# Kernel tuning notes

Hardware: AMD Instinct MI355X
Metric: run time of the kernel (lower is better)

Reference implementation:

```python
import jax, jax.numpy as jnp
import numpy as np

N_QUBITS = 6

def _apply_1q(state, U, w):
    # state: [B] + [2]*6 complex; U: [2,2] complex
    ax = 1 + w
    s = jnp.moveaxis(state, ax, -1)
    s = jnp.einsum('...j,ij->...i', s, U)
    return jnp.moveaxis(s, -1, ax)

def _apply_cnot(state, ctrl, tgt):
    ca, ta = 1 + ctrl, 1 + tgt
    s = jnp.moveaxis(state, (ca, ta), (1, 2))  # [B,2,2,...]
    s = jnp.stack([s[:, 0], s[:, 1, ::-1]], axis=1)
    return jnp.moveaxis(s, (1, 2), (ca, ta))

def _rot(phi, theta, omega):
    # PennyLane Rot = RZ(omega) RY(theta) RZ(phi)
    c, s = jnp.cos(theta / 2), jnp.sin(theta / 2)
    return jnp.stack([
        jnp.stack([jnp.exp(-0.5j * (phi + omega)) * c, -jnp.exp(0.5j * (phi - omega)) * s]),
        jnp.stack([jnp.exp(-0.5j * (phi - omega)) * s, jnp.exp(0.5j * (phi + omega)) * c]),
    ])

def _quantum(xq, qw):
    B = xq.shape[0]
    # AngleEmbedding RY: product state, per-qubit amplitudes [cos(x/2), sin(x/2)]
    amps = jnp.stack([jnp.cos(xq / 2), jnp.sin(xq / 2)], axis=-1)  # [B,6,2]
    state = amps[:, 0]
    for i in range(1, N_QUBITS):
        state = jnp.einsum('b...,bj->b...j', state, amps[:, i])
    state = state.astype(jnp.complex64)  # [B,2,2,2,2,2,2]
    # StronglyEntanglingLayers: per layer Rot on each wire, then CNOT ring of range r
    n_layers = qw.shape[0]
    for l in range(n_layers):
        for w in range(N_QUBITS):
            U = _rot(qw[l, w, 0], qw[l, w, 1], qw[l, w, 2])
            state = _apply_1q(state, U, w)
        r = (l % (N_QUBITS - 1)) + 1  # default ranges
        for w in range(N_QUBITS):
            state = _apply_cnot(state, w, (w + r) % N_QUBITS)
    probs = jnp.abs(state) ** 2
    zs = []
    for w in range(N_QUBITS):
        axes = tuple(a for a in range(1, N_QUBITS + 1) if a != 1 + w)
        p = jnp.sum(probs, axis=axes)  # [B,2]
        zs.append(p[:, 0] - p[:, 1])
    return jnp.stack(zs, axis=-1)  # [B,6]

def setup_inputs() -> dict:
    key = jax.random.key(0)
    ks = jax.random.split(key, 10)
    B = 16384
    return {
        'xc': jax.random.normal(ks[0], (B, 2048), jnp.float32),
        'xq': jax.random.uniform(ks[1], (B, N_QUBITS), jnp.float32),
        'W1': jax.random.normal(ks[2], (64, 2048), jnp.float32) * 0.02,
        'b1': jnp.zeros((64,), jnp.float32),
        'qw': jax.random.uniform(ks[3], (3, N_QUBITS, 3), jnp.float32, 0.0, 2 * np.pi),
        'Wq': jax.random.normal(ks[4], (16, N_QUBITS), jnp.float32) * 0.3,
        'bq': jnp.zeros((16,), jnp.float32),
        'Wf': jax.random.normal(ks[5], (3, 80), jnp.float32) * 0.1,
        'bf': jnp.zeros((3,), jnp.float32),
    }

def reference(xc, xq, W1, b1, qw, Wq, bq, Wf, bf):
    c = jax.nn.relu(xc @ W1.T + b1)                 # [B,64]
    q = _quantum(xq, qw) @ Wq.T + bq                # [B,16]
    return jnp.concatenate([c, q], axis=1) @ Wf.T + bf  # [B,3]
```

## Files before the change

### kernel.cpp

```cpp
#include <hip/hip_runtime.h>
#include <hip/hip_bf16.h>

#define NQ 6

typedef __attribute__((ext_vector_type(8))) short short8;
typedef __attribute__((ext_vector_type(4))) float floatx4;

#define WS_MQ_F   8192
#define WS_CQ_F   (8192+18)
#define WS_W1BF_B 36864

__global__ __launch_bounds__(64) void prep_kernel(
    const float* __restrict__ qw, int n_layers,
    const float* __restrict__ W1, const float* __restrict__ Wq,
    const float* __restrict__ bq, const float* __restrict__ Wf,
    const float* __restrict__ bf, float* __restrict__ ws_f,
    short* __restrict__ w1bf)
{
    const int blk  = blockIdx.x;
    const int lane = threadIdx.x;

    if (blk == 0) {
        if (lane < 18) {
            int j = lane / 6, wi = lane % 6;
            float s = 0.f;
            for (int m = 0; m < 16; ++m) s += Wf[j*80 + 64 + m] * Wq[m*6 + wi];
            ws_f[WS_MQ_F + lane] = s;
        } else if (lane < 21) {
            int j = lane - 18;
            float s = bf[j];
            for (int m = 0; m < 16; ++m) s += Wf[j*80 + 64 + m] * bq[m];
            ws_f[WS_CQ_F + j] = s;
        }
    } else if (blk <= 64) {
        const int j = blk - 1;
        float re = (lane == j) ? 1.f : 0.f;
        float im = 0.f;
        for (int l = 0; l < n_layers; ++l) {
            for (int w = 0; w < NQ; ++w) {
                const float* g = qw + (l*NQ + w)*3;
                float phi = g[0], th = g[1], om = g[2];
                float c, s;  __sincosf(0.5f*th, &s, &c);
                float sa, ca; __sincosf(0.5f*(phi+om), &sa, &ca);
                float sb, cb; __sincosf(0.5f*(phi-om), &sb, &cb);
                float u00r =  c*ca, u00i = -c*sa;
                float u01r = -s*cb, u01i = -s*sb;
                float u10r =  s*cb, u10i = -s*sb;
                float u11r =  c*ca, u11i =  c*sa;
                int p = 5 - w, mask = 1 << p;
                float pre = __shfl_xor(re, mask, 64);
                float pim = __shfl_xor(im, mask, 64);
                int b = (lane >> p) & 1;
                float mr = b ? u11r : u00r, mi = b ? u11i : u00i;
                float pr = b ? u10r : u01r, pi = b ? u10i : u01i;
                float nre = mr*re - mi*im + pr*pre - pi*pim;
                float nim = mr*im + mi*re + pr*pim + pi*pre;
                re = nre; im = nim;
            }
            int r = l % (NQ-1) + 1;
            for (int w = 0; w < NQ; ++w) {
                int tgt = (w + r) % NQ;
                int tmask = 1 << (5 - tgt);
                float pre = __shfl_xor(re, tmask, 64);
                float pim = __shfl_xor(im, tmask, 64);
                int cs = (lane >> (5 - w)) & 1;
                re = cs ? pre : re;
                im = cs ? pim : im;
            }
        }
        ws_f[(lane*64 + j)*2 + 0] = re;
        ws_f[(lane*64 + j)*2 + 1] = im;
    } else {
        int idx = (blk - 65)*512 + lane*8;
        if (idx < 64*2048) {
            float4 a0 = *(const float4*)(W1 + idx);
            float4 a1 = *(const float4*)(W1 + idx + 4);
            union { short8 v; __hip_bfloat162 h[4]; } u;
            float2 f;
            f.x=a0.x; f.y=a0.y; u.h[0] = __float22bfloat162_rn(f);
            f.x=a0.z; f.y=a0.w; u.h[1] = __float22bfloat162_rn(f);
            f.x=a1.x; f.y=a1.y; u.h[2] = __float22bfloat162_rn(f);
            f.x=a1.z; f.y=a1.w; u.h[3] = __float22bfloat162_rn(f);
            *(short8*)(w1bf + idx) = u.v;
        }
    }
}

__global__ __launch_bounds__(256) void fused_kernel(
    const float* __restrict__ xq, const float2* __restrict__ U,
    const float* __restrict__ ws_f,
    const float* __restrict__ xc, const short* __restrict__ w1bf,
    const float* __restrict__ b1, const float* __restrict__ Wf,
    float* __restrict__ out)
{
    const int tid  = threadIdx.x;
    const int lane = tid & 63;
    const int t    = __builtin_amdgcn_readfirstlane((int)(tid >> 6));
    const int blk  = blockIdx.x;

    __shared__ float zbuf[4][64][6];
    __shared__ float qres[64][3];
    __shared__ float cl[64][65];

    {
        const int b = blk*64 + lane;
        float a[64];
        const float* x = xq + (size_t)b*6;
        a[0] = 1.f;
        #pragma unroll
        for (int q = 0; q < 6; ++q) {
            float c, s; __sincosf(0.5f*x[q], &s, &c);
            const int sz = 1 << q;
            #pragma unroll
            for (int m = sz-1; m >= 0; --m) {
                float v = a[m];
                a[2*m+1] = v*s;
                a[2*m+0] = v*c;
            }
        }

        float zp[6] = {0,0,0,0,0,0};
        const float2* Urow = U + t*16*64;
        for (int ii = 0; ii < 16; ++ii) {
            float rr = 0.f, ri = 0.f;
            #pragma unroll
            for (int j = 0; j < 64; ++j) {
                float2 u = Urow[ii*64 + j];
                rr += u.x * a[j];
                ri += u.y * a[j];
            }
            float p = rr*rr + ri*ri;
            int i = t*16 + ii;
            #pragma unroll
            for (int w = 0; w < 6; ++w) zp[w] += ((i >> (5-w)) & 1) ? -p : p;
        }
        #pragma unroll
        for (int w = 0; w < 6; ++w) zbuf[t][lane][w] = zp[w];
    }
    __syncthreads();
    if (t == 0) {
        float z[6];
        #pragma unroll
        for (int w = 0; w < 6; ++w)
            z[w] = zbuf[0][lane][w] + zbuf[1][lane][w] + zbuf[2][lane][w] + zbuf[3][lane][w];
        #pragma unroll
        for (int j = 0; j < 3; ++j) {
            float v = ws_f[WS_CQ_F + j];
            #pragma unroll
            for (int w = 0; w < 6; ++w) v += ws_f[WS_MQ_F + j*6 + w] * z[w];
            qres[lane][j] = v;
        }
    }

    const int row  = blk*64 + t*16 + (lane & 15);
    const int koff = (lane >> 4) * 8;

    const float* ap = xc + (size_t)row*2048 + koff;
    const short* bp = w1bf + (lane & 15)*2048 + koff;

    floatx4 acc0 = {0,0,0,0}, acc1 = {0,0,0,0}, acc2 = {0,0,0,0}, acc3 = {0,0,0,0};

    float4 a0  = *(const float4*)ap;
    float4 a1  = *(const float4*)(ap + 4);
    short8 b0  = *(const short8*)(bp);
    short8 bv1 = *(const short8*)(bp + 16*2048);
    short8 b2  = *(const short8*)(bp + 32*2048);
    short8 b3  = *(const short8*)(bp + 48*2048);

    #pragma unroll 4
    for (int kk = 1; kk < 64; ++kk) {
        const float* apn = ap + kk*32;
        const short* bpn = bp + kk*32;
        float4 na0 = *(const float4*)apn;
        float4 na1 = *(const float4*)(apn + 4);
        short8 nb0 = *(const short8*)(bpn);
        short8 nb1 = *(const short8*)(bpn + 16*2048);
        short8 nb2 = *(const short8*)(bpn + 32*2048);
        short8 nb3 = *(const short8*)(bpn + 48*2048);

        union { short8 v; __hip_bfloat162 h[4]; } af;
        float2 f;
        f.x=a0.x; f.y=a0.y; af.h[0] = __float22bfloat162_rn(f);
        f.x=a0.z; f.y=a0.w; af.h[1] = __float22bfloat162_rn(f);
        f.x=a1.x; f.y=a1.y; af.h[2] = __float22bfloat162_rn(f);
        f.x=a1.z; f.y=a1.w; af.h[3] = __float22bfloat162_rn(f);

        acc0 = __builtin_amdgcn_mfma_f32_16x16x32_bf16(af.v, b0,  acc0, 0, 0, 0);
        acc1 = __builtin_amdgcn_mfma_f32_16x16x32_bf16(af.v, bv1, acc1, 0, 0, 0);
        acc2 = __builtin_amdgcn_mfma_f32_16x16x32_bf16(af.v, b2,  acc2, 0, 0, 0);
        acc3 = __builtin_amdgcn_mfma_f32_16x16x32_bf16(af.v, b3,  acc3, 0, 0, 0);

        a0 = na0; a1 = na1; b0 = nb0; bv1 = nb1; b2 = nb2; b3 = nb3;
    }
    {
        union { short8 v; __hip_bfloat162 h[4]; } af;
        float2 f;
        f.x=a0.x; f.y=a0.y; af.h[0] = __float22bfloat162_rn(f);
        f.x=a0.z; f.y=a0.w; af.h[1] = __float22bfloat162_rn(f);
        f.x=a1.x; f.y=a1.y; af.h[2] = __float22bfloat162_rn(f);
        f.x=a1.z; f.y=a1.w; af.h[3] = __float22bfloat162_rn(f);
        acc0 = __builtin_amdgcn_mfma_f32_16x16x32_bf16(af.v, b0,  acc0, 0, 0, 0);
        acc1 = __builtin_amdgcn_mfma_f32_16x16x32_bf16(af.v, bv1, acc1, 0, 0, 0);
        acc2 = __builtin_amdgcn_mfma_f32_16x16x32_bf16(af.v, b2,  acc2, 0, 0, 0);
        acc3 = __builtin_amdgcn_mfma_f32_16x16x32_bf16(af.v, b3,  acc3, 0, 0, 0);
    }

    const int rbase = t*16 + ((lane >> 4) * 4);
    const int c0 = lane & 15;
    float bb0 = b1[c0], bb1 = b1[16 + c0], bb2 = b1[32 + c0], bb3 = b1[48 + c0];
    #pragma unroll
    for (int r = 0; r < 4; ++r) {
        cl[rbase + r][ 0 + c0] = fmaxf(acc0[r] + bb0, 0.f);
        cl[rbase + r][16 + c0] = fmaxf(acc1[r] + bb1, 0.f);
        cl[rbase + r][32 + c0] = fmaxf(acc2[r] + bb2, 0.f);
        cl[rbase + r][48 + c0] = fmaxf(acc3[r] + bb3, 0.f);
    }
    __syncthreads();

    const int rr2 = tid & 63;
    if (t < 3) {
        float v = 0.f;
        #pragma unroll
        for (int col = 0; col < 64; ++col) v += Wf[t*80 + col] * cl[rr2][col];
        int g = blk*64 + rr2;
        out[(size_t)g*3 + t] = v + qres[rr2][t];
    }
}

extern "C" void kernel_launch(void* const* d_in, const int* in_sizes, int n_in,
                              void* d_out, int out_size, void* d_ws, size_t ws_size,
                              hipStream_t stream) {
    const float* xc = (const float*)d_in[0];
    const float* xq = (const float*)d_in[1];
    const float* W1 = (const float*)d_in[2];
    const float* b1 = (const float*)d_in[3];
    const float* qw = (const float*)d_in[4];
    const float* Wq = (const float*)d_in[5];
    const float* bq = (const float*)d_in[6];
    const float* Wf = (const float*)d_in[7];
    const float* bf = (const float*)d_in[8];
    float* out = (float*)d_out;

    const int B = in_sizes[1] / NQ;
    const int n_layers = in_sizes[4] / (NQ * 3);

    char* ws = (char*)d_ws;
    float*  ws_f  = (float*)ws;
    float2* U     = (float2*)ws;
    short*  w1bf  = (short*)(ws + WS_W1BF_B);

    prep_kernel<<<dim3(321), dim3(64), 0, stream>>>(qw, n_layers, W1, Wq, bq, Wf, bf, ws_f, w1bf);
    fused_kernel<<<dim3(B/64), dim3(256), 0, stream>>>(xq, U, ws_f, xc, w1bf, b1, Wf, out);
}
```

Baseline: 245.2 us.

## Split fused kernel into 16 waves with one 16x16 MFMA tile each

Grows the fused block from 4 to 16 waves. The quantum statevector rows are split 4 per wave instead of 16, and the 64x64 linear-layer tile is split so each wave computes one 16x16 output tile with a single accumulator instead of four. With only 256 blocks, the aim is more resident waves per CU to hide load and MFMA latency and to shorten each wave's serial quantum loop. In exchange, each xc row slice is now loaded by four waves instead of one, relying on cache for reuse. The 1024-thread launch bound also caps registers per thread, which may spill the 64-float amplitude array.

```diff
diff --git a/kernel.cpp b/kernel.cpp
--- a/kernel.cpp
+++ b/kernel.cpp
@@ -86,7 +86,7 @@
     }
 }
 
-__global__ __launch_bounds__(256) void fused_kernel(
+__global__ __launch_bounds__(1024) void fused_kernel(
     const float* __restrict__ xq, const float2* __restrict__ U,
     const float* __restrict__ ws_f,
     const float* __restrict__ xc, const short* __restrict__ w1bf,
@@ -98,7 +98,7 @@
     const int t    = __builtin_amdgcn_readfirstlane((int)(tid >> 6));
     const int blk  = blockIdx.x;
 
-    __shared__ float zbuf[4][64][6];
+    __shared__ float zbuf[16][64][6];
     __shared__ float qres[64][3];
     __shared__ float cl[64][65];
 
@@ -120,8 +120,8 @@
         }
 
         float zp[6] = {0,0,0,0,0,0};
-        const float2* Urow = U + t*16*64;
-        for (int ii = 0; ii < 16; ++ii) {
+        const float2* Urow = U + t*4*64;
+        for (int ii = 0; ii < 4; ++ii) {
             float rr = 0.f, ri = 0.f;
             #pragma unroll
             for (int j = 0; j < 64; ++j) {
@@ -130,7 +130,7 @@
                 ri += u.y * a[j];
             }
             float p = rr*rr + ri*ri;
-            int i = t*16 + ii;
+            int i = t*4 + ii;
             #pragma unroll
             for (int w = 0; w < 6; ++w) zp[w] += ((i >> (5-w)) & 1) ? -p : p;
         }
@@ -141,8 +141,12 @@
     if (t == 0) {
         float z[6];
         #pragma unroll
-        for (int w = 0; w < 6; ++w)
-            z[w] = zbuf[0][lane][w] + zbuf[1][lane][w] + zbuf[2][lane][w] + zbuf[3][lane][w];
+        for (int w = 0; w < 6; ++w) {
+            float s = 0.f;
+            #pragma unroll
+            for (int sbi = 0; sbi < 16; ++sbi) s += zbuf[sbi][lane][w];
+            z[w] = s;
+        }
         #pragma unroll
         for (int j = 0; j < 3; ++j) {
             float v = ws_f[WS_CQ_F + j];
@@ -152,31 +156,24 @@
         }
     }
 
-    const int row  = blk*64 + t*16 + (lane & 15);
+    const int wr = t >> 2, wc = t & 3;
+    const int row  = blk*64 + wr*16 + (lane & 15);
     const int koff = (lane >> 4) * 8;
 
     const float* ap = xc + (size_t)row*2048 + koff;
-    const short* bp = w1bf + (lane & 15)*2048 + koff;
-
-    floatx4 acc0 = {0,0,0,0}, acc1 = {0,0,0,0}, acc2 = {0,0,0,0}, acc3 = {0,0,0,0};
-
-    float4 a0  = *(const float4*)ap;
-    float4 a1  = *(const float4*)(ap + 4);
-    short8 b0  = *(const short8*)(bp);
-    short8 bv1 = *(const short8*)(bp + 16*2048);
-    short8 b2  = *(const short8*)(bp + 32*2048);
-    short8 b3  = *(const short8*)(bp + 48*2048);
+    const short* bp = w1bf + (wc*16 + (lane & 15))*2048 + koff;
+
+    floatx4 acc = {0,0,0,0};
+
+    float4 a0 = *(const float4*)ap;
+    float4 a1 = *(const float4*)(ap + 4);
+    short8 bv = *(const short8*)bp;
 
     #pragma unroll 4
     for (int kk = 1; kk < 64; ++kk) {
-        const float* apn = ap + kk*32;
-        const short* bpn = bp + kk*32;
-        float4 na0 = *(const float4*)apn;
-        float4 na1 = *(const float4*)(apn + 4);
-        short8 nb0 = *(const short8*)(bpn);
-        short8 nb1 = *(const short8*)(bpn + 16*2048);
-        short8 nb2 = *(const short8*)(bpn + 32*2048);
-        short8 nb3 = *(const short8*)(bpn + 48*2048);
+        float4 na0 = *(const float4*)(ap + kk*32);
+        float4 na1 = *(const float4*)(ap + kk*32 + 4);
+        short8 nbv = *(const short8*)(bp + kk*32);
 
         union { short8 v; __hip_bfloat162 h[4]; } af;
         float2 f;
@@ -185,12 +182,9 @@
         f.x=a1.x; f.y=a1.y; af.h[2] = __float22bfloat162_rn(f);
         f.x=a1.z; f.y=a1.w; af.h[3] = __float22bfloat162_rn(f);
 
-        acc0 = __builtin_amdgcn_mfma_f32_16x16x32_bf16(af.v, b0,  acc0, 0, 0, 0);
-        acc1 = __builtin_amdgcn_mfma_f32_16x16x32_bf16(af.v, bv1, acc1, 0, 0, 0);
-        acc2 = __builtin_amdgcn_mfma_f32_16x16x32_bf16(af.v, b2,  acc2, 0, 0, 0);
-        acc3 = __builtin_amdgcn_mfma_f32_16x16x32_bf16(af.v, b3,  acc3, 0, 0, 0);
-
-        a0 = na0; a1 = na1; b0 = nb0; bv1 = nb1; b2 = nb2; b3 = nb3;
+        acc = __builtin_amdgcn_mfma_f32_16x16x32_bf16(af.v, bv, acc, 0, 0, 0);
+
+        a0 = na0; a1 = na1; bv = nbv;
     }
     {
         union { short8 v; __hip_bfloat162 h[4]; } af;
@@ -199,22 +193,15 @@
         f.x=a0.z; f.y=a0.w; af.h[1] = __float22bfloat162_rn(f);
         f.x=a1.x; f.y=a1.y; af.h[2] = __float22bfloat162_rn(f);
         f.x=a1.z; f.y=a1.w; af.h[3] = __float22bfloat162_rn(f);
-        acc0 = __builtin_amdgcn_mfma_f32_16x16x32_bf16(af.v, b0,  acc0, 0, 0, 0);
-        acc1 = __builtin_amdgcn_mfma_f32_16x16x32_bf16(af.v, bv1, acc1, 0, 0, 0);
-        acc2 = __builtin_amdgcn_mfma_f32_16x16x32_bf16(af.v, b2,  acc2, 0, 0, 0);
-        acc3 = __builtin_amdgcn_mfma_f32_16x16x32_bf16(af.v, b3,  acc3, 0, 0, 0);
-    }
-
-    const int rbase = t*16 + ((lane >> 4) * 4);
-    const int c0 = lane & 15;
-    float bb0 = b1[c0], bb1 = b1[16 + c0], bb2 = b1[32 + c0], bb3 = b1[48 + c0];
+        acc = __builtin_amdgcn_mfma_f32_16x16x32_bf16(af.v, bv, acc, 0, 0, 0);
+    }
+
+    const int rbase = wr*16 + ((lane >> 4) * 4);
+    const int c0 = wc*16 + (lane & 15);
+    const float bb = b1[c0];
     #pragma unroll
-    for (int r = 0; r < 4; ++r) {
-        cl[rbase + r][ 0 + c0] = fmaxf(acc0[r] + bb0, 0.f);
-        cl[rbase + r][16 + c0] = fmaxf(acc1[r] + bb1, 0.f);
-        cl[rbase + r][32 + c0] = fmaxf(acc2[r] + bb2, 0.f);
-        cl[rbase + r][48 + c0] = fmaxf(acc3[r] + bb3, 0.f);
-    }
+    for (int r = 0; r < 4; ++r)
+        cl[rbase + r][c0] = fmaxf(acc[r] + bb, 0.f);
     __syncthreads();
 
     const int rr2 = tid & 63;
@@ -250,5 +237,5 @@
     short*  w1bf  = (short*)(ws + WS_W1BF_B);
 
     prep_kernel<<<dim3(321), dim3(64), 0, stream>>>(qw, n_layers, W1, Wq, bq, Wf, bf, ws_f, w1bf);
-    fused_kernel<<<dim3(B/64), dim3(256), 0, stream>>>(xq, U, ws_f, xc, w1bf, b1, Wf, out);
+    fused_kernel<<<dim3(B/64), dim3(1024), 0, stream>>>(xq, U, ws_f, xc, w1bf, b1, Wf, out);
 }
```

Result: slower. 270.8 us (+10.4%).
